# Kernel tuning notes

Measured on AMD Instinct MI355X. Metric: run time of the kernel, lower is better.

## Reference

```python
import jax, jax.numpy as jnp
import numpy as np

D = 768; NH = 12; DH = 64; DEPTH = 12; P = 16; IMG = 224; NC = 1000; DFF = 3072
GAMMA = 0.01; MIN_TOKENS = 16; EPS = 1e-6
SCALE = DH ** -0.5
NPATCH = (IMG // P) ** 2  # 196


def _ln(x, w, b, eps=1e-6):
    mu = x.mean(-1, keepdims=True)
    var = ((x - mu) ** 2).mean(-1, keepdims=True)
    return (x - mu) * jax.lax.rsqrt(var + eps) * w + b


def _block(x, p):
    # one pre-norm ViT block; returns new x, attention matrix A [B,H,T,T], values v [B,H,T,DH]
    (l1w, l1b, qw, qb, pw, pb, l2w, l2b, f1w, f1b, f2w, f2b) = p
    B, T, _ = x.shape
    qkv = _ln(x, l1w, l1b) @ qw + qb                      # [B,T,3D]
    qkv = qkv.reshape(B, T, 3, NH, DH).transpose(2, 0, 3, 1, 4)
    q, k, v = qkv[0], qkv[1], qkv[2]                      # [B,H,T,DH]
    A = jax.nn.softmax(jnp.einsum('bhtd,bhsd->bhts', q, k) * SCALE, axis=-1)
    out = jnp.einsum('bhts,bhsd->bhtd', A, v).transpose(0, 2, 1, 3).reshape(B, T, NH * DH)
    x = x + out @ pw + pb
    h = jax.nn.gelu(_ln(x, l2w, l2b) @ f1w + f1b, approximate=False)
    x = x + h @ f2w + f2b
    return x, A, v


def _embed(x, patch_w, patch_b, cls_token, pos_embed):
    B = x.shape[0]
    feat = jax.lax.conv_general_dilated(x, patch_w, (P, P), 'VALID',
                                        dimension_numbers=('NCHW', 'OIHW', 'NCHW'))  # [B,D,14,14]
    feat = feat.reshape(B, D, -1).transpose(0, 2, 1) + patch_b                       # [B,196,D]
    cls = jnp.broadcast_to(cls_token, (B, 1, D))
    return jnp.concatenate([cls, feat], axis=1) + pos_embed                          # [B,197,D]


def setup_inputs() -> dict:
    key = jax.random.key(0)
    ks = jax.random.split(key, 12)
    s = 0.02
    n = lambda k, shape: jax.random.normal(k, shape, jnp.float32) * s
    return {
        'x': jax.random.normal(ks[0], (32, 3, IMG, IMG), jnp.float32),
        'patch_w': n(ks[1], (D, 3, P, P)),
        'patch_b': jnp.zeros((D,), jnp.float32),
        'cls_token': n(ks[2], (1, 1, D)),
        'pos_embed': n(ks[3], (1, NPATCH + 1, D)),
        'ln1_w': jnp.ones((DEPTH, D), jnp.float32),
        'ln1_b': jnp.zeros((DEPTH, D), jnp.float32),
        'qkv_w': n(ks[4], (DEPTH, D, 3 * D)),
        'qkv_b': jnp.zeros((DEPTH, 3 * D), jnp.float32),
        'proj_w': n(ks[5], (DEPTH, D, D)),
        'proj_b': jnp.zeros((DEPTH, D), jnp.float32),
        'ln2_w': jnp.ones((DEPTH, D), jnp.float32),
        'ln2_b': jnp.zeros((DEPTH, D), jnp.float32),
        'fc1_w': n(ks[6], (DEPTH, D, DFF)),
        'fc1_b': jnp.zeros((DEPTH, DFF), jnp.float32),
        'fc2_w': n(ks[7], (DEPTH, DFF, D)),
        'fc2_b': jnp.zeros((DEPTH, D), jnp.float32),
        'norm_w': jnp.ones((D,), jnp.float32),
        'norm_b': jnp.zeros((D,), jnp.float32),
        'head_w': n(ks[8], (D, NC)),
        'head_b': jnp.zeros((NC,), jnp.float32),
    }


def reference(x, patch_w, patch_b, cls_token, pos_embed, ln1_w, ln1_b, qkv_w, qkv_b,
              proj_w, proj_b, ln2_w, ln2_b, fc1_w, fc1_b, fc2_w, fc2_b,
              norm_w, norm_b, head_w, head_b):
    # NOTE: token pruning produces data-dependent shapes, so this runs eagerly
    # (Python control flow on concrete values), exactly mirroring the torch code.
    x = _embed(x, patch_w, patch_b, cls_token, pos_embed)
    N = x.shape[1] - 1
    prev_mass = None
    for l in range(DEPTH):
        p = (ln1_w[l], ln1_b[l], qkv_w[l], qkv_b[l], proj_w[l], proj_b[l],
             ln2_w[l], ln2_b[l], fc1_w[l], fc1_b[l], fc2_w[l], fc2_b[l])
        x, A, v = _block(x, p)
        if N <= MIN_TOKENS:
            continue
        Am = A.mean(axis=1)                                   # [B,T,T] head-mean attention
        Vm = v.mean(axis=1)                                   # [B,T,DH] head-mean values
        rho = (1.0 + Am[:, 0, 0] * jnp.linalg.norm(Vm[:, 0], axis=-1)).mean()
        A_cls = Am[:, 0, 1:N + 1]                             # [B,N] cls->patch attention
        V_pt = Vm[:, 1:N + 1]
        Vc = V_pt - V_pt.mean(axis=1, keepdims=True)
        Vn = jnp.linalg.norm(Vc, axis=-1)                     # [B,N]
        mu = Vn.mean(axis=1, keepdims=True)
        sd = Vn.std(axis=1, keepdims=True, ddof=1)            # torch.std is unbiased
        J = A_cls * jax.nn.relu((Vn - mu) / (sd + EPS))       # [B,N] Jacobian score
        mass = J.sum(axis=1).mean()
        if prev_mass is not None:
            eta = mass / (prev_mass + EPS)
            keep_ratio = jnp.clip(rho * eta, 0.25, 4.0) ** (-GAMMA)
            N_next = max(MIN_TOKENS, int(N * float(keep_ratio)))
        else:
            N_next = N
        if N_next < N:
            idx = jnp.sort(jax.lax.top_k(J.mean(axis=0), N_next)[1]) + 1
            keep = jnp.concatenate([jnp.zeros((1,), idx.dtype), idx])
            x = x[:, keep]
            N = N_next
        prev_mass = mass
    x = _ln(x, norm_w, norm_b)
    return x[:, 0] @ head_w + head_b
```

## Files before the change

kernel.cpp:

```cpp
#include <hip/hip_runtime.h>
#include <math.h>

#define D 768
#define NH 12
#define DH 64
#define DEPTH 12
#define TMAX 197
#define NPATCH 196
#define BATCH 32
#define DFF 3072
#define NC 1000
#define QSTRIDE 2304
#define SCALE 0.125f
#define EPSF 1e-6f
#define MPAD 6400

typedef __bf16 bf16x8 __attribute__((ext_vector_type(8)));
typedef float f32x4 __attribute__((ext_vector_type(4)));
typedef short sshort8 __attribute__((ext_vector_type(8)));


__device__ __forceinline__ short f2bf(float x) {
  unsigned u = __float_as_uint(x);
  u = u + 0x7fffu + ((u >> 16) & 1u);
  return (short)(u >> 16);
}
__device__ __forceinline__ float bf2f(short h) {
  return __uint_as_float(((unsigned)(unsigned short)h) << 16);
}
__device__ __forceinline__ void bsplit(float x, short* hp, short* lp) {
  short h = f2bf(x);
  *hp = h;
  *lp = f2bf(x - bf2f(h));
}

__device__ __forceinline__ void gll16(const void* g, void* l) {
  __builtin_amdgcn_global_load_lds(
      (const __attribute__((address_space(1))) void*)g,
      (__attribute__((address_space(3))) void*)l, 16, 0, 0);
}


__device__ __forceinline__ float block_reduce_sum(float v, float* red, int tid) {
  red[tid] = v; __syncthreads();
  #pragma unroll
  for (int o = 128; o > 0; o >>= 1) { if (tid < o) red[tid] += red[tid + o]; __syncthreads(); }
  float r = red[0]; __syncthreads();
  return r;
}

__global__ void fail_kernel(float* out) { out[0] = 1.0e6f; }

__global__ void init_kernel(int* si, float* sf) {
  si[0] = TMAX;
  si[1] = 0;
  si[2] = 0;
  sf[0] = 0.f;
}

__global__ void wsplit_t(const float* __restrict__ W, short* __restrict__ Wpk,
                         int K, int N) {
  __shared__ float t[32][33];
  int n0 = blockIdx.x * 32, k0 = blockIdx.y * 32;
  int tid = threadIdx.x;
  int kk = tid >> 3, n4 = (tid & 7) * 4;
  float4 v = *(const float4*)(W + (size_t)(k0 + kk) * N + n0 + n4);
  t[kk][n4] = v.x; t[kk][n4 + 1] = v.y; t[kk][n4 + 2] = v.z; t[kk][n4 + 3] = v.w;
  __syncthreads();
  int nn = tid >> 3, k4 = (tid & 7) * 4;
  short* dh = Wpk + (size_t)(n0 + nn) * 2 * K + k0 + k4;
  short* dl = dh + K;
  #pragma unroll
  for (int c = 0; c < 4; ++c) bsplit(t[k4 + c][nn], &dh[c], &dl[c]);
}

__global__ void wsplit_nt(const float* __restrict__ W, short* __restrict__ Wpk, int K) {
  const float* src = W + (size_t)blockIdx.x * K;
  short* dh = Wpk + (size_t)blockIdx.x * 2 * K;
  short* dl = dh + K;
  for (int k = threadIdx.x; k < K; k += 256) bsplit(src[k], &dh[k], &dl[k]);
}


__global__ void im2col_kernel(const float* __restrict__ x, short* __restrict__ Impk) {
  int p = blockIdx.x, b = blockIdx.y;
  int py = p / 14, px = p % 14;
  short* dst = Impk + ((size_t)b * NPATCH + p) * 1536;
  for (int k = threadIdx.x; k < D; k += 256) {
    int c = k >> 8; int rem = k & 255; int i = rem >> 4; int j = rem & 15;
    float v = x[(((size_t)b * 3 + c) * 224 + py * 16 + i) * 224 + px * 16 + j];
    bsplit(v, &dst[k], &dst[768 + k]);
  }
}

__global__ void assemble_kernel(const float* __restrict__ PE, const float* __restrict__ cls,
                                const float* __restrict__ pos, float* __restrict__ X) {
  int t = blockIdx.x, b = blockIdx.y; int tid = threadIdx.x;
  float* xp = X + ((size_t)(b * TMAX) + t) * D;
  for (int k = tid; k < D; k += 256) {
    float v = (t == 0) ? cls[k] : PE[((size_t)(b * NPATCH) + (t - 1)) * D + k];
    xp[k] = v + pos[(size_t)t * D + k];
  }
}


__global__ void ln_kernel(const float* __restrict__ Xin, short* __restrict__ XNpk,
                          const float* __restrict__ wgt, const float* __restrict__ bsh,
                          const int* __restrict__ si) {
  int row = blockIdx.x;
  if ((row % TMAX) >= si[0]) return;
  __shared__ float red[256];
  int tid = threadIdx.x;
  const float* xp = Xin + (size_t)row * D;
  float v0 = xp[tid], v1 = xp[tid + 256], v2 = xp[tid + 512];
  float mu = block_reduce_sum(v0 + v1 + v2, red, tid) * (1.0f / 768.0f);
  float d0 = v0 - mu, d1 = v1 - mu, d2 = v2 - mu;
  float var = block_reduce_sum(d0 * d0 + d1 * d1 + d2 * d2, red, tid) * (1.0f / 768.0f);
  float inv = 1.0f / sqrtf(var + EPSF);
  short* op = XNpk + (size_t)row * 1536;
  float y0 = d0 * inv * wgt[tid] + bsh[tid];
  float y1 = d1 * inv * wgt[tid + 256] + bsh[tid + 256];
  float y2 = d2 * inv * wgt[tid + 512] + bsh[tid + 512];
  bsplit(y0, &op[tid], &op[768 + tid]);
  bsplit(y1, &op[tid + 256], &op[768 + tid + 256]);
  bsplit(y2, &op[tid + 512], &op[768 + tid + 512]);
}

__global__ void lnfinal_kernel(const float* __restrict__ X, float* __restrict__ CLSb,
                               const float* __restrict__ wgt, const float* __restrict__ bsh) {
  int b = blockIdx.x; int tid = threadIdx.x;
  __shared__ float red[256];
  const float* xp = X + (size_t)b * TMAX * D;
  float v0 = xp[tid], v1 = xp[tid + 256], v2 = xp[tid + 512];
  float mu = block_reduce_sum(v0 + v1 + v2, red, tid) * (1.0f / 768.0f);
  float d0 = v0 - mu, d1 = v1 - mu, d2 = v2 - mu;
  float var = block_reduce_sum(d0 * d0 + d1 * d1 + d2 * d2, red, tid) * (1.0f / 768.0f);
  float inv = 1.0f / sqrtf(var + EPSF);
  float* op = CLSb + (size_t)b * D;
  op[tid]       = d0 * inv * wgt[tid]       + bsh[tid];
  op[tid + 256] = d1 * inv * wgt[tid + 256] + bsh[tid + 256];
  op[tid + 512] = d2 * inv * wgt[tid + 512] + bsh[tid + 512];
}

__device__ __forceinline__ void swz_map(int d, int nx, int ny, int wsub,
                                        int& bx, int& by) {
  int q = ny >> 3, r = ny & 7;
  int rows, mb, l;
  int big = (q + 1) * nx;
  if (d < r * big) { int c = d / big; l = d - c * big; rows = q + 1; mb = c * (q + 1); }
  else { int d2 = d - r * big; int sm = q * nx; int c2 = d2 / sm; l = d2 - c2 * sm; rows = q; mb = r * (q + 1) + c2 * q; }
  int wspan = wsub * rows;
  int j = l / wspan; int t = l - j * wspan;
  int ml = t / wsub; int dx = t - ml * wsub;
  bx = j * wsub + dx; by = mb + ml;
}


#define GTM 128
#define GTN 128
#define GTK 32

template<int EPI, int SWZ>
__global__ __launch_bounds__(256)
void mgemm_kernel(const short* __restrict__ Apk, const short* __restrict__ Bpk,
                  const float* __restrict__ bias, const float* __restrict__ Rsrc,
                  float* __restrict__ Cf, short* __restrict__ Cpk,
                  int M, int K, int N, int nx, int ny, int wsub) {
  __shared__ char lds[65536];
  const int tid = threadIdx.x;
  const int ln = tid & 63;
  const int wv = tid >> 6;
  const int wm = wv >> 1, wn = wv & 1;

  int bx, by;
  if (SWZ) swz_map(blockIdx.x, nx, ny, wsub, bx, by);
  else { bx = blockIdx.x % nx; by = blockIdx.x / nx; }

  const int m0 = by * GTM, n0 = bx * GTN;
  const int lm = ln & 15, kc = ln >> 4;
  const size_t rs = 2 * (size_t)K;

  f32x4 acc[4][4];
  f32x4 zv = {0.f, 0.f, 0.f, 0.f};
  #pragma unroll
  for (int i = 0; i < 4; ++i)
    #pragma unroll
    for (int j = 0; j < 4; ++j) acc[i][j] = zv;

  auto stage = [&](int k0, int buf) {
    char* base = lds + (buf << 15);
    #pragma unroll
    for (int i = 0; i < 4; ++i) {
      int s = (i << 8) + tid;
      int r = s >> 3;
      int sl = (s & 7) ^ (r & 7);
      size_t eoff = (size_t)(sl >> 2) * K + (size_t)(k0 + ((sl & 3) << 3));
      int ldsoff = ((i << 8) + (tid & 192)) << 4;
      gll16(Apk + (size_t)(m0 + r) * rs + eoff, base + ldsoff);
      gll16(Bpk + (size_t)(n0 + r) * rs + eoff, base + 16384 + ldsoff);
    }
  };

  const int nk = K / GTK;
  stage(0, 0);
  for (int kt = 0; kt < nk; ++kt) {
    if (kt + 1 < nk) {
      stage((kt + 1) * GTK, (kt + 1) & 1);
      asm volatile("s_waitcnt vmcnt(8)" ::: "memory");
    } else {
      asm volatile("s_waitcnt vmcnt(0)" ::: "memory");
    }
    __builtin_amdgcn_s_barrier();
    __builtin_amdgcn_sched_barrier(0);

    const char* pa = lds + ((kt & 1) << 15);
    const char* pb = pa + 16384;
    bf16x8 bh[4], bl[4];
    #pragma unroll
    for (int j = 0; j < 4; ++j) {
      int c = wn * 64 + j * 16 + lm;
      int bo = c * 128 + ((kc ^ (c & 7)) << 4);
      bh[j] = *(const bf16x8*)(pb + bo);
      bl[j] = *(const bf16x8*)(pb + (bo ^ 64));
    }
    #pragma unroll
    for (int i = 0; i < 4; ++i) {
      int r = wm * 64 + i * 16 + lm;
      int ao = r * 128 + ((kc ^ (r & 7)) << 4);
      bf16x8 ah = *(const bf16x8*)(pa + ao);
      bf16x8 al = *(const bf16x8*)(pa + (ao ^ 64));
      #pragma unroll
      for (int j = 0; j < 4; ++j) {
        acc[i][j] = __builtin_amdgcn_mfma_f32_16x16x32_bf16(ah, bh[j], acc[i][j], 0, 0, 0);
        acc[i][j] = __builtin_amdgcn_mfma_f32_16x16x32_bf16(ah, bl[j], acc[i][j], 0, 0, 0);
        acc[i][j] = __builtin_amdgcn_mfma_f32_16x16x32_bf16(al, bh[j], acc[i][j], 0, 0, 0);
      }
    }
    if (kt + 1 < nk)
      __builtin_amdgcn_s_barrier();
  }

  #pragma unroll
  for (int i = 0; i < 4; ++i) {
    #pragma unroll
    for (int t = 0; t < 4; ++t) {
      int m = m0 + wm * 64 + i * 16 + kc * 4 + t;
      if (m >= M) continue;
      #pragma unroll
      for (int j = 0; j < 4; ++j) {
        int n = n0 + wn * 64 + j * 16 + lm;
        float v = acc[i][j][t] + bias[n];
        if (EPI == 1) v += Rsrc[(size_t)m * N + n];
        if (EPI == 2) {
          v = v * 0.5f * (1.0f + erff(v * 0.70710678118654752f));
          short h = f2bf(v);
          Cpk[(size_t)m * 2 * N + n] = h;
          Cpk[(size_t)m * 2 * N + N + n] = f2bf(v - bf2f(h));
        } else {
          Cf[(size_t)m * N + n] = v;
        }
      }
    }
  }
}


#define BM 128
#define BN 64
#define BK 16

__global__ __launch_bounds__(256, 2)
void gemm_kernel(const float* __restrict__ A, const float* __restrict__ Bw,
                 const float* __restrict__ bias, float* __restrict__ C,
                 int M, int K, int N) {
  __shared__ float As[BK][BM + 4];
  __shared__ float Bs[BK][BN];
  int tid = threadIdx.x;
  int tx = tid & 15;
  int ty = tid >> 4;
  int m0 = blockIdx.y * BM;
  int n0 = blockIdx.x * BN;
  float acc[8][4];
  #pragma unroll
  for (int i = 0; i < 8; ++i)
    #pragma unroll
    for (int j = 0; j < 4; ++j) acc[i][j] = 0.f;
  const int lkA = tid & 15;
  const int lmA = tid >> 4;
  const int lnB = tid & 63;
  const int lkB = tid >> 6;
  for (int k0 = 0; k0 < K; k0 += BK) {
    #pragma unroll
    for (int r = 0; r < 8; ++r) {
      int ml = r * 16 + lmA;
      int m = m0 + ml;
      float va = 0.f;
      if (m < M) va = A[(size_t)m * K + k0 + lkA];
      As[lkA][ml] = va;
    }
    #pragma unroll
    for (int r = 0; r < 4; ++r) {
      int kk = r * 4 + lkB;
      int n = n0 + lnB;
      float vb = 0.f;
      if (n < N) vb = Bw[(size_t)(k0 + kk) * N + n];
      Bs[kk][lnB] = vb;
    }
    __syncthreads();
    #pragma unroll
    for (int kk = 0; kk < BK; ++kk) {
      const float4 b4 = *(const float4*)(&Bs[kk][tx * 4]);
      const float4 a0 = *(const float4*)(&As[kk][ty * 8]);
      const float4 a1 = *(const float4*)(&As[kk][ty * 8 + 4]);
      const float a[8] = {a0.x, a0.y, a0.z, a0.w, a1.x, a1.y, a1.z, a1.w};
      const float bb[4] = {b4.x, b4.y, b4.z, b4.w};
      #pragma unroll
      for (int i = 0; i < 8; ++i)
        #pragma unroll
        for (int j = 0; j < 4; ++j)
          acc[i][j] = fmaf(a[i], bb[j], acc[i][j]);
    }
    __syncthreads();
  }
  #pragma unroll
  for (int i = 0; i < 8; ++i) {
    int m = m0 + ty * 8 + i;
    if (m >= M) continue;
    #pragma unroll
    for (int j = 0; j < 4; ++j) {
      int n = n0 + tx * 4 + j;
      if (n >= N) continue;
      C[(size_t)m * N + n] = acc[i][j] + bias[n];
    }
  }
}


#define QT 64
#define KVT 64

__global__ __launch_bounds__(256)
void mattn_kernel(const float* __restrict__ QKV, short* __restrict__ AOpk,
                  const int* __restrict__ si) {
  const int tok = si[0];
  const int bh = blockIdx.x; const int b = bh / NH, h = bh % NH;
  const int q0 = blockIdx.y * QT;
  if (q0 >= tok) return;
  __shared__ short Kh[4096], Kl[4096], Vth[4096], Vtl[4096];
  __shared__ short Pb[8192];
  const int tid = threadIdx.x;
  const int l = tid & 63, w = tid >> 6;
  const int lm = l & 15, lg = l >> 4;

  bf16x8 qh[2], ql[2];
  {
    int qrow = q0 + w * 16 + lm;
    if (qrow >= TMAX) qrow = TMAX - 1;
    const float* qp = QKV + (size_t)(b * TMAX + qrow) * QSTRIDE + h * DH + lg * 8;
    #pragma unroll
    for (int c = 0; c < 2; ++c) {
      sshort8 hs, ls;
      #pragma unroll
      for (int j = 0; j < 8; ++j) {
        float v = qp[c * 32 + j];
        short hh = f2bf(v);
        hs[j] = hh;
        ls[j] = f2bf(v - bf2f(hh));
      }
      qh[c] = __builtin_bit_cast(bf16x8, hs);
      ql[c] = __builtin_bit_cast(bf16x8, ls);
    }
  }

  float mrun[4], lrun[4];
  f32x4 oacc[4];
  f32x4 zv = {0.f, 0.f, 0.f, 0.f};
  #pragma unroll
  for (int t = 0; t < 4; ++t) { mrun[t] = -1e30f; lrun[t] = 0.f; }
  #pragma unroll
  for (int j = 0; j < 4; ++j) oacc[j] = zv;

  const int r0 = (tid >> 4) * 4;
  const int td4 = (tid & 15) * 4;

  for (int j0 = 0; j0 < tok; j0 += KVT) {
    {
      float vbuf[16];
      #pragma unroll
      for (int i = 0; i < 4; ++i) {
        int gr = j0 + r0 + i; if (gr >= TMAX) gr = TMAX - 1;
        const float* kp = QKV + (size_t)(b * TMAX + gr) * QSTRIDE + D + h * DH + td4;
        float4 kv = *(const float4*)kp;
        short4 sh, sl;
        sh.x = f2bf(kv.x); sl.x = f2bf(kv.x - bf2f(sh.x));
        sh.y = f2bf(kv.y); sl.y = f2bf(kv.y - bf2f(sh.y));
        sh.z = f2bf(kv.z); sl.z = f2bf(kv.z - bf2f(sh.z));
        sh.w = f2bf(kv.w); sl.w = f2bf(kv.w - bf2f(sh.w));
        int r = r0 + i;
        int so = r * 64 + (((td4 >> 3) ^ (r & 7)) << 3) + (td4 & 7);
        *(short4*)(Kh + so) = sh;
        *(short4*)(Kl + so) = sl;
        const float* vp = QKV + (size_t)(b * TMAX + gr) * QSTRIDE + 2 * D + h * DH + td4;
        float4 vv = *(const float4*)vp;
        vbuf[i * 4 + 0] = vv.x; vbuf[i * 4 + 1] = vv.y;
        vbuf[i * 4 + 2] = vv.z; vbuf[i * 4 + 3] = vv.w;
      }
      #pragma unroll
      for (int dd = 0; dd < 4; ++dd) {
        int d = td4 + dd;
        short4 sh, sl;
        float c0 = vbuf[dd], c1 = vbuf[4 + dd], c2 = vbuf[8 + dd], c3 = vbuf[12 + dd];
        sh.x = f2bf(c0); sl.x = f2bf(c0 - bf2f(sh.x));
        sh.y = f2bf(c1); sl.y = f2bf(c1 - bf2f(sh.y));
        sh.z = f2bf(c2); sl.z = f2bf(c2 - bf2f(sh.z));
        sh.w = f2bf(c3); sl.w = f2bf(c3 - bf2f(sh.w));
        int so = d * 64 + (((r0 >> 3) ^ (d & 7)) << 3) + (r0 & 7);
        *(short4*)(Vth + so) = sh;
        *(short4*)(Vtl + so) = sl;
      }
    }
    __syncthreads();

    f32x4 sacc[4];
    #pragma unroll
    for (int jk = 0; jk < 4; ++jk) sacc[jk] = zv;
    #pragma unroll
    for (int c = 0; c < 2; ++c) {
      #pragma unroll
      for (int jk = 0; jk < 4; ++jk) {
        int row = jk * 16 + lm;
        int so = row * 64 + (((c * 4 + lg) ^ (row & 7)) << 3);
        bf16x8 kbh = *(const bf16x8*)(Kh + so);
        bf16x8 kbl = *(const bf16x8*)(Kl + so);
        sacc[jk] = __builtin_amdgcn_mfma_f32_16x16x32_bf16(qh[c], kbh, sacc[jk], 0, 0, 0);
        sacc[jk] = __builtin_amdgcn_mfma_f32_16x16x32_bf16(qh[c], kbl, sacc[jk], 0, 0, 0);
        sacc[jk] = __builtin_amdgcn_mfma_f32_16x16x32_bf16(ql[c], kbh, sacc[jk], 0, 0, 0);
      }
    }

    float p[4][4];
    #pragma unroll
    for (int jk = 0; jk < 4; ++jk) {
      bool valid = (j0 + jk * 16 + lm) < tok;
      #pragma unroll
      for (int t = 0; t < 4; ++t)
        p[jk][t] = valid ? sacc[jk][t] * SCALE : -1e30f;
    }
    float mt[4], mnew[4], co[4], rsm[4];
    #pragma unroll
    for (int t = 0; t < 4; ++t) {
      mt[t] = fmaxf(fmaxf(p[0][t], p[1][t]), fmaxf(p[2][t], p[3][t]));
      #pragma unroll
      for (int off = 1; off < 16; off <<= 1)
        mt[t] = fmaxf(mt[t], __shfl_xor(mt[t], off, 16));
      mnew[t] = fmaxf(mrun[t], mt[t]);
      co[t] = expf(mrun[t] - mnew[t]);
      rsm[t] = 0.f;
    }
    #pragma unroll
    for (int jk = 0; jk < 4; ++jk)
      #pragma unroll
      for (int t = 0; t < 4; ++t) {
        p[jk][t] = expf(p[jk][t] - mnew[t]);
        rsm[t] += p[jk][t];
      }
    #pragma unroll
    for (int t = 0; t < 4; ++t) {
      #pragma unroll
      for (int off = 1; off < 16; off <<= 1)
        rsm[t] += __shfl_xor(rsm[t], off, 16);
      lrun[t] = lrun[t] * co[t] + rsm[t];
      mrun[t] = mnew[t];
    }
    #pragma unroll
    for (int jd = 0; jd < 4; ++jd)
      #pragma unroll
      for (int t = 0; t < 4; ++t) oacc[jd][t] *= co[t];

    short* Pw = Pb + w * 2048;
    #pragma unroll
    for (int jk = 0; jk < 4; ++jk)
      #pragma unroll
      for (int t = 0; t < 4; ++t) {
        int q = lg * 4 + t;
        int col = jk * 16 + lm;
        short hh = f2bf(p[jk][t]);
        short hl = f2bf(p[jk][t] - bf2f(hh));
        int so = q * 64 + (((col >> 3) ^ (q & 7)) << 3) + (col & 7);
        Pw[so] = hh;
        Pw[1024 + so] = hl;
      }

    #pragma unroll
    for (int c = 0; c < 2; ++c) {
      int aro = lm * 64 + (((c * 4 + lg) ^ (lm & 7)) << 3);
      bf16x8 pah = *(const bf16x8*)(Pw + aro);
      bf16x8 pal = *(const bf16x8*)(Pw + 1024 + aro);
      #pragma unroll
      for (int jd = 0; jd < 4; ++jd) {
        int d = jd * 16 + lm;
        int so = d * 64 + (((c * 4 + lg) ^ (d & 7)) << 3);
        bf16x8 vbh = *(const bf16x8*)(Vth + so);
        bf16x8 vbl = *(const bf16x8*)(Vtl + so);
        oacc[jd] = __builtin_amdgcn_mfma_f32_16x16x32_bf16(pah, vbh, oacc[jd], 0, 0, 0);
        oacc[jd] = __builtin_amdgcn_mfma_f32_16x16x32_bf16(pah, vbl, oacc[jd], 0, 0, 0);
        oacc[jd] = __builtin_amdgcn_mfma_f32_16x16x32_bf16(pal, vbh, oacc[jd], 0, 0, 0);
      }
    }
    __syncthreads();
  }

  #pragma unroll
  for (int t = 0; t < 4; ++t) {
    int q = q0 + w * 16 + lg * 4 + t;
    if (q >= tok) continue;
    float inv = 1.0f / lrun[t];
    short* op = AOpk + (size_t)(b * TMAX + q) * 1536 + h * DH;
    #pragma unroll
    for (int jd = 0; jd < 4; ++jd) {
      int d = jd * 16 + lm;
      float y = oacc[jd][t] * inv;
      short hh = f2bf(y);
      op[d] = hh;
      op[768 + d] = f2bf(y - bf2f(hh));
    }
  }
}

__global__ void clsrow_kernel(const float* __restrict__ QKV, float* __restrict__ Pcls,
                              const int* __restrict__ si) {
  int tok = si[0];
  int bh = blockIdx.x; int b = bh / NH, h = bh % NH;
  int tid = threadIdx.x;
  __shared__ float q[DH];
  __shared__ float red[256];
  if (tid < DH) q[tid] = QKV[((size_t)(b * TMAX)) * QSTRIDE + h * DH + tid];
  __syncthreads();
  float sval = -1e30f;
  if (tid < tok) {
    const float* kp = QKV + ((size_t)(b * TMAX) + tid) * QSTRIDE + D + h * DH;
    float a = 0.f;
    #pragma unroll
    for (int dd = 0; dd < DH; ++dd) a = fmaf(q[dd], kp[dd], a);
    sval = a * SCALE;
  }
  red[tid] = sval; __syncthreads();
  #pragma unroll
  for (int o = 128; o > 0; o >>= 1) { if (tid < o) red[tid] = fmaxf(red[tid], red[tid + o]); __syncthreads(); }
  float mx = red[0]; __syncthreads();
  float e = (tid < tok) ? expf(sval - mx) : 0.f;
  red[tid] = e; __syncthreads();
  #pragma unroll
  for (int o = 128; o > 0; o >>= 1) { if (tid < o) red[tid] += red[tid + o]; __syncthreads(); }
  if (tid < tok) Pcls[(size_t)bh * TMAX + tid] = e / red[0];
}

__global__ void aclsmean_kernel(const float* __restrict__ Pcls, float* __restrict__ Acls,
                                const int* __restrict__ si) {
  int tok = si[0]; int b = blockIdx.x; int tid = threadIdx.x;
  if (tid < tok) {
    float s = 0.f;
    #pragma unroll
    for (int h = 0; h < NH; ++h) s += Pcls[((size_t)b * NH + h) * TMAX + tid];
    Acls[b * TMAX + tid] = s * (1.0f / 12.0f);
  }
}

__global__ void vmean_kernel(const float* __restrict__ QKV, float* __restrict__ Vm,
                             const int* __restrict__ si) {
  int tok = si[0];
  int t = blockIdx.x, b = blockIdx.y;
  if (t >= tok) return;
  int d = threadIdx.x;
  const float* vp = QKV + ((size_t)(b * TMAX + t)) * QSTRIDE + 2 * D;
  float s = 0.f;
  #pragma unroll
  for (int h = 0; h < NH; ++h) s += vp[h * DH + d];
  Vm[((size_t)b * TMAX + t) * DH + d] = s * (1.0f / 12.0f);
}


__global__ void stats_kernel(const float* __restrict__ Vm, const float* __restrict__ Acls,
                             float* __restrict__ Jbuf, float* __restrict__ Jsum,
                             float* __restrict__ rhot, const int* __restrict__ si) {
  int tok = si[0]; int N = tok - 1;
  if (N <= 16) return;
  int b = blockIdx.x; int tid = threadIdx.x;
  __shared__ float red[256];
  __shared__ float vmean[DH];
  __shared__ float Vn[NPATCH];
  const float* vb = Vm + (size_t)b * TMAX * DH;

  float x0 = 0.f;
  if (tid < DH) { float v = vb[tid]; x0 = v * v; }
  red[tid] = x0; __syncthreads();
  #pragma unroll
  for (int o = 128; o > 0; o >>= 1) { if (tid < o) red[tid] += red[tid + o]; __syncthreads(); }
  if (tid == 0) rhot[b] = 1.0f + Acls[b * TMAX] * sqrtf(red[0]);
  __syncthreads();

  int d = tid & 63, part = tid >> 6;
  float s = 0.f;
  for (int t = 1 + part; t <= N; t += 4) s += vb[(size_t)t * DH + d];
  red[tid] = s; __syncthreads();
  if (tid < DH) vmean[tid] = (red[tid] + red[tid + 64] + red[tid + 128] + red[tid + 192]) / (float)N;
  __syncthreads();

  if (tid < N) {
    const float* vp = vb + (size_t)(tid + 1) * DH;
    float a = 0.f;
    #pragma unroll
    for (int dd = 0; dd < DH; ++dd) { float z = vp[dd] - vmean[dd]; a = fmaf(z, z, a); }
    Vn[tid] = sqrtf(a);
  }
  __syncthreads();

  red[tid] = (tid < N) ? Vn[tid] : 0.f; __syncthreads();
  #pragma unroll
  for (int o = 128; o > 0; o >>= 1) { if (tid < o) red[tid] += red[tid + o]; __syncthreads(); }
  float mu = red[0] / (float)N;
  __syncthreads();
  float dv = (tid < N) ? (Vn[tid] - mu) : 0.f;
  red[tid] = dv * dv; __syncthreads();
  #pragma unroll
  for (int o = 128; o > 0; o >>= 1) { if (tid < o) red[tid] += red[tid + o]; __syncthreads(); }
  float sd = sqrtf(red[0] / (float)(N - 1));
  __syncthreads();

  float Jv = 0.f;
  if (tid < N) {
    float z = (Vn[tid] - mu) / (sd + EPSF);
    z = fmaxf(z, 0.f);
    Jv = Acls[b * TMAX + 1 + tid] * z;
    Jbuf[b * NPATCH + tid] = Jv;
  }
  red[tid] = Jv; __syncthreads();
  #pragma unroll
  for (int o = 128; o > 0; o >>= 1) { if (tid < o) red[tid] += red[tid + o]; __syncthreads(); }
  if (tid == 0) Jsum[b] = red[0];
}

__global__ void decide_kernel(const float* __restrict__ Jbuf, const float* __restrict__ Jsum,
                              const float* __restrict__ rhot, int* __restrict__ keep,
                              int* __restrict__ si, float* __restrict__ sf) {
  int tok = si[0]; int N = tok - 1;
  int tid = threadIdx.x;
  if (N <= 16) { if (tid == 0) si[2] = 0; return; }
  __shared__ float red[256];
  __shared__ float Jms[NPATCH];
  __shared__ int sel[NPATCH];

  red[tid] = (tid < BATCH) ? rhot[tid] : 0.f; __syncthreads();
  #pragma unroll
  for (int o = 128; o > 0; o >>= 1) { if (tid < o) red[tid] += red[tid + o]; __syncthreads(); }
  float rho = red[0] / (float)BATCH; __syncthreads();
  red[tid] = (tid < BATCH) ? Jsum[tid] : 0.f; __syncthreads();
  #pragma unroll
  for (int o = 128; o > 0; o >>= 1) { if (tid < o) red[tid] += red[tid + o]; __syncthreads(); }
  float mass = red[0] / (float)BATCH;
  int prev_valid = si[1];
  float prev = sf[0];
  __syncthreads();

  int N_next = N;
  if (prev_valid) {
    float eta = mass / (prev + EPSF);
    float re = rho * eta;
    re = fminf(fmaxf(re, 0.25f), 4.0f);
    double kr = pow((double)re, -0.01);
    int nn = (int)((double)N * kr);
    N_next = nn > 16 ? nn : 16;
  }
  if (tid == 0) { si[1] = 1; sf[0] = mass; }

  if (N_next < N) {
    if (tid < N) {
      float sJ = 0.f;
      for (int bb = 0; bb < BATCH; ++bb) sJ += Jbuf[bb * NPATCH + tid];
      Jms[tid] = sJ / (float)BATCH;
    }
    __syncthreads();
    if (tid < N) {
      float me = Jms[tid]; int rank = 0;
      for (int s2 = 0; s2 < N; ++s2) {
        float ov = Jms[s2];
        if (ov > me || (ov == me && s2 < tid)) ++rank;
      }
      sel[tid] = (rank < N_next) ? 1 : 0;
    }
    __syncthreads();
    if (tid == 0) {
      int c = 0; keep[c++] = 0;
      for (int t2 = 0; t2 < N; ++t2) if (sel[t2]) keep[c++] = t2 + 1;
      si[0] = N_next + 1;
      si[2] = 1;
    }
  } else {
    if (tid == 0) si[2] = 0;
  }
}

__global__ void gather_kernel(const float* __restrict__ X, float* __restrict__ T,
                              const int* __restrict__ keep, const int* __restrict__ si) {
  if (!si[2]) return;
  int tok = si[0];
  int i = blockIdx.x, b = blockIdx.y;
  if (i >= tok) return;
  int src = keep[i];
  const float* xp = X + ((size_t)(b * TMAX) + src) * D;
  float* tp = T + ((size_t)(b * TMAX) + i) * D;
  int tid = threadIdx.x;
  tp[tid] = xp[tid]; tp[tid + 256] = xp[tid + 256]; tp[tid + 512] = xp[tid + 512];
}

__global__ void copyback_kernel(const float* __restrict__ T, float* __restrict__ X,
                                const int* __restrict__ si) {
  if (!si[2]) return;
  int tok = si[0];
  int i = blockIdx.x, b = blockIdx.y;
  if (i >= tok) return;
  const float* tp = T + ((size_t)(b * TMAX) + i) * D;
  float* xp = X + ((size_t)(b * TMAX) + i) * D;
  int tid = threadIdx.x;
  xp[tid] = tp[tid]; xp[tid + 256] = tp[tid + 256]; xp[tid + 512] = tp[tid + 512];
}


extern "C" void kernel_launch(void* const* d_in, const int* in_sizes, int n_in,
                              void* d_out, int out_size, void* d_ws, size_t ws_size,
                              hipStream_t stream) {
  (void)in_sizes; (void)n_in; (void)out_size;
  const float* x       = (const float*)d_in[0];
  const float* patch_w = (const float*)d_in[1];
  const float* patch_b = (const float*)d_in[2];
  const float* cls_tok = (const float*)d_in[3];
  const float* pos     = (const float*)d_in[4];
  const float* ln1w    = (const float*)d_in[5];
  const float* ln1b    = (const float*)d_in[6];
  const float* qkvw    = (const float*)d_in[7];
  const float* qkvb    = (const float*)d_in[8];
  const float* projw   = (const float*)d_in[9];
  const float* projb   = (const float*)d_in[10];
  const float* ln2w    = (const float*)d_in[11];
  const float* ln2b    = (const float*)d_in[12];
  const float* fc1w    = (const float*)d_in[13];
  const float* fc1b    = (const float*)d_in[14];
  const float* fc2w    = (const float*)d_in[15];
  const float* fc2b    = (const float*)d_in[16];
  const float* normw   = (const float*)d_in[17];
  const float* normb   = (const float*)d_in[18];
  const float* headw   = (const float*)d_in[19];
  const float* headb   = (const float*)d_in[20];
  float* out = (float*)d_out;

  char* w = (char*)d_ws;
  size_t off = 0;
  auto alloc = [&](size_t bytes) -> void* {
    void* p = w + off;
    off += (bytes + 255) & ~(size_t)255;
    return p;
  };
  const size_t MROWS = (size_t)BATCH * TMAX;
  float* X    = (float*)alloc(MROWS * D * 4);
  short* XNpk = (short*)alloc((size_t)MPAD * 1536 * 2);
  float* QKV  = (float*)alloc(MROWS * QSTRIDE * 4);
  short* AOpk = (short*)alloc((size_t)MPAD * 1536 * 2);
  short* Hpk  = (short*)alloc((size_t)MPAD * 2 * DFF * 2);
  float* Vm   = (float*)alloc(MROWS * DH * 4);
  float* Pcls = (float*)alloc((size_t)BATCH * NH * TMAX * 4);
  float* Acls = (float*)alloc((size_t)BATCH * TMAX * 4);
  float* Jbuf = (float*)alloc((size_t)BATCH * NPATCH * 4);
  float* Jsum = (float*)alloc(BATCH * 4);
  float* rhot = (float*)alloc(BATCH * 4);
  int*   keep = (int*)alloc(256 * 4);
  int*   si   = (int*)alloc(64 * 4);
  float* sf   = (float*)alloc(64 * 4);
  float* CLS  = (float*)alloc((size_t)BATCH * D * 4);
  short* Wq   = (short*)alloc((size_t)QSTRIDE * 2 * D * 2);
  short* Wp   = (short*)alloc((size_t)D * 2 * D * 2);
  short* W1   = (short*)alloc((size_t)DFF * 2 * D * 2);
  short* W2   = (short*)alloc((size_t)D * 2 * DFF * 2);
  short* Wpat = (short*)alloc((size_t)D * 2 * D * 2);
  short* Impk = Hpk;
  float* TMP  = (float*)Hpk;
  float* Ef32 = QKV;

  if (off > ws_size) {
    fail_kernel<<<1, 1, 0, stream>>>(out);
    return;
  }

  init_kernel<<<1, 1, 0, stream>>>(si, sf);

  im2col_kernel<<<dim3(NPATCH, BATCH), 256, 0, stream>>>(x, Impk);
  wsplit_nt<<<D, 256, 0, stream>>>(patch_w, Wpat, D);
  mgemm_kernel<0, 1><<<6 * 49, 256, 0, stream>>>(
      Impk, Wpat, patch_b, nullptr, Ef32, nullptr, BATCH * NPATCH, D, D, 6, 49, 6);
  assemble_kernel<<<dim3(TMAX, BATCH), 256, 0, stream>>>(Ef32, cls_tok, pos, X);

  for (int l = 0; l < DEPTH; ++l) {
    const float* l1w = ln1w + l * D;
    const float* l1b = ln1b + l * D;
    const float* qw  = qkvw + (size_t)l * D * 3 * D;
    const float* qb  = qkvb + (size_t)l * 3 * D;
    const float* pw  = projw + (size_t)l * D * D;
    const float* pb  = projb + (size_t)l * D;
    const float* l2w = ln2w + l * D;
    const float* l2b = ln2b + l * D;
    const float* f1w = fc1w + (size_t)l * D * DFF;
    const float* f1b = fc1b + (size_t)l * DFF;
    const float* f2w = fc2w + (size_t)l * DFF * D;
    const float* f2b = fc2b + (size_t)l * D;

    wsplit_t<<<dim3(QSTRIDE / 32, D / 32), 256, 0, stream>>>(qw, Wq, D, QSTRIDE);
    wsplit_t<<<dim3(D / 32, D / 32), 256, 0, stream>>>(pw, Wp, D, D);
    wsplit_t<<<dim3(DFF / 32, D / 32), 256, 0, stream>>>(f1w, W1, D, DFF);
    wsplit_t<<<dim3(D / 32, DFF / 32), 256, 0, stream>>>(f2w, W2, DFF, D);

    ln_kernel<<<BATCH * TMAX, 256, 0, stream>>>(X, XNpk, l1w, l1b, si);
    mgemm_kernel<0, 1><<<18 * 50, 256, 0, stream>>>(
        XNpk, Wq, qb, nullptr, QKV, nullptr, (int)MROWS, D, QSTRIDE, 18, 50, 6);
    mattn_kernel<<<dim3(BATCH * NH, (TMAX + QT - 1) / QT), 256, 0, stream>>>(QKV, AOpk, si);
    clsrow_kernel<<<BATCH * NH, 256, 0, stream>>>(QKV, Pcls, si);
    aclsmean_kernel<<<BATCH, 256, 0, stream>>>(Pcls, Acls, si);
    vmean_kernel<<<dim3(TMAX, BATCH), 64, 0, stream>>>(QKV, Vm, si);
    mgemm_kernel<1, 1><<<6 * 50, 256, 0, stream>>>(
        AOpk, Wp, pb, X, X, nullptr, (int)MROWS, D, D, 6, 50, 6);
    ln_kernel<<<BATCH * TMAX, 256, 0, stream>>>(X, XNpk, l2w, l2b, si);
    mgemm_kernel<2, 1><<<24 * 50, 256, 0, stream>>>(
        XNpk, W1, f1b, nullptr, nullptr, Hpk, (int)MROWS, D, DFF, 24, 50, 8);
    mgemm_kernel<1, 0><<<6 * 50, 256, 0, stream>>>(
        Hpk, W2, f2b, X, X, nullptr, (int)MROWS, DFF, D, 6, 50, 6);
    stats_kernel<<<BATCH, 256, 0, stream>>>(Vm, Acls, Jbuf, Jsum, rhot, si);
    decide_kernel<<<1, 256, 0, stream>>>(Jbuf, Jsum, rhot, keep, si, sf);
    gather_kernel<<<dim3(TMAX, BATCH), 256, 0, stream>>>(X, TMP, keep, si);
    copyback_kernel<<<dim3(TMAX, BATCH), 256, 0, stream>>>(TMP, X, si);
  }

  lnfinal_kernel<<<BATCH, 256, 0, stream>>>(X, CLS, normw, normb);
  gemm_kernel<<<dim3(16, 1), 256, 0, stream>>>(CLS, headw, headb, out, BATCH, D, NC);
}
```

Before: 6.730 ms.

## Emit QKV as pre-split bf16 hi/lo pairs and simplify GEMM pipeline sync

The QKV GEMM gains a new epilogue that writes each output as a bf16 hi/lo pair. The attention, cls-row and v-mean kernels then read those pairs directly instead of splitting fp32 values on every load. The GEMM main loop also swaps its hand-placed vmcnt waits and split barriers for a single __syncthreads before staging the next tile, which may reduce how much load latency overlaps with compute. Clsrow and vmean now rebuild fp32 from hi+lo, a small precision change. The embedding output buffer is aliased onto AOpk.

```diff
diff --git a/kernel.cpp b/kernel.cpp
--- a/kernel.cpp
+++ b/kernel.cpp
@@ -11,6 +11,7 @@
 #define DFF 3072
 #define NC 1000
 #define QSTRIDE 2304
+#define QPK 4608
 #define SCALE 0.125f
 #define EPSF 1e-6f
 #define MPAD 6400
@@ -204,15 +205,8 @@
   const int nk = K / GTK;
   stage(0, 0);
   for (int kt = 0; kt < nk; ++kt) {
-    if (kt + 1 < nk) {
-      stage((kt + 1) * GTK, (kt + 1) & 1);
-      asm volatile("s_waitcnt vmcnt(8)" ::: "memory");
-    } else {
-      asm volatile("s_waitcnt vmcnt(0)" ::: "memory");
-    }
-    __builtin_amdgcn_s_barrier();
-    __builtin_amdgcn_sched_barrier(0);
-
+    __syncthreads();
+    if (kt + 1 < nk) stage((kt + 1) * GTK, (kt + 1) & 1);
     const char* pa = lds + ((kt & 1) << 15);
     const char* pb = pa + 16384;
     bf16x8 bh[4], bl[4];
@@ -236,8 +230,6 @@
         acc[i][j] = __builtin_amdgcn_mfma_f32_16x16x32_bf16(al, bh[j], acc[i][j], 0, 0, 0);
       }
     }
-    if (kt + 1 < nk)
-      __builtin_amdgcn_s_barrier();
   }
 
   #pragma unroll
@@ -251,8 +243,8 @@
         int n = n0 + wn * 64 + j * 16 + lm;
         float v = acc[i][j][t] + bias[n];
         if (EPI == 1) v += Rsrc[(size_t)m * N + n];
-        if (EPI == 2) {
-          v = v * 0.5f * (1.0f + erff(v * 0.70710678118654752f));
+        if (EPI == 2 || EPI == 3) {
+          if (EPI == 2) v = v * 0.5f * (1.0f + erff(v * 0.70710678118654752f));
           short h = f2bf(v);
           Cpk[(size_t)m * 2 * N + n] = h;
           Cpk[(size_t)m * 2 * N + N + n] = f2bf(v - bf2f(h));
@@ -340,7 +332,7 @@
 #define KVT 64
 
 __global__ __launch_bounds__(256)
-void mattn_kernel(const float* __restrict__ QKV, short* __restrict__ AOpk,
+void mattn_kernel(const short* __restrict__ QKVpk, short* __restrict__ AOpk,
                   const int* __restrict__ si) {
   const int tok = si[0];
   const int bh = blockIdx.x; const int b = bh / NH, h = bh % NH;
@@ -356,19 +348,11 @@
   {
     int qrow = q0 + w * 16 + lm;
     if (qrow >= TMAX) qrow = TMAX - 1;
-    const float* qp = QKV + (size_t)(b * TMAX + qrow) * QSTRIDE + h * DH + lg * 8;
+    const short* qp = QKVpk + (size_t)(b * TMAX + qrow) * QPK + h * DH + lg * 8;
     #pragma unroll
     for (int c = 0; c < 2; ++c) {
-      sshort8 hs, ls;
-      #pragma unroll
-      for (int j = 0; j < 8; ++j) {
-        float v = qp[c * 32 + j];
-        short hh = f2bf(v);
-        hs[j] = hh;
-        ls[j] = f2bf(v - bf2f(hh));
-      }
-      qh[c] = __builtin_bit_cast(bf16x8, hs);
-      ql[c] = __builtin_bit_cast(bf16x8, ls);
+      qh[c] = __builtin_bit_cast(bf16x8, *(const sshort8*)(qp + c * 32));
+      ql[c] = __builtin_bit_cast(bf16x8, *(const sshort8*)(qp + QSTRIDE + c * 32));
     }
   }
 
@@ -385,35 +369,28 @@
 
   for (int j0 = 0; j0 < tok; j0 += KVT) {
     {
-      float vbuf[16];
+      short vh[16], vl[16];
       #pragma unroll
       for (int i = 0; i < 4; ++i) {
         int gr = j0 + r0 + i; if (gr >= TMAX) gr = TMAX - 1;
-        const float* kp = QKV + (size_t)(b * TMAX + gr) * QSTRIDE + D + h * DH + td4;
-        float4 kv = *(const float4*)kp;
-        short4 sh, sl;
-        sh.x = f2bf(kv.x); sl.x = f2bf(kv.x - bf2f(sh.x));
-        sh.y = f2bf(kv.y); sl.y = f2bf(kv.y - bf2f(sh.y));
-        sh.z = f2bf(kv.z); sl.z = f2bf(kv.z - bf2f(sh.z));
-        sh.w = f2bf(kv.w); sl.w = f2bf(kv.w - bf2f(sh.w));
+        const short* bp = QKVpk + (size_t)(b * TMAX + gr) * QPK;
+        short4 kh4 = *(const short4*)(bp + D + h * DH + td4);
+        short4 kl4 = *(const short4*)(bp + D + QSTRIDE + h * DH + td4);
         int r = r0 + i;
         int so = r * 64 + (((td4 >> 3) ^ (r & 7)) << 3) + (td4 & 7);
-        *(short4*)(Kh + so) = sh;
-        *(short4*)(Kl + so) = sl;
-        const float* vp = QKV + (size_t)(b * TMAX + gr) * QSTRIDE + 2 * D + h * DH + td4;
-        float4 vv = *(const float4*)vp;
-        vbuf[i * 4 + 0] = vv.x; vbuf[i * 4 + 1] = vv.y;
-        vbuf[i * 4 + 2] = vv.z; vbuf[i * 4 + 3] = vv.w;
+        *(short4*)(Kh + so) = kh4;
+        *(short4*)(Kl + so) = kl4;
+        short4 vh4 = *(const short4*)(bp + 2 * D + h * DH + td4);
+        short4 vl4 = *(const short4*)(bp + 2 * D + QSTRIDE + h * DH + td4);
+        vh[i * 4 + 0] = vh4.x; vh[i * 4 + 1] = vh4.y; vh[i * 4 + 2] = vh4.z; vh[i * 4 + 3] = vh4.w;
+        vl[i * 4 + 0] = vl4.x; vl[i * 4 + 1] = vl4.y; vl[i * 4 + 2] = vl4.z; vl[i * 4 + 3] = vl4.w;
       }
       #pragma unroll
       for (int dd = 0; dd < 4; ++dd) {
         int d = td4 + dd;
         short4 sh, sl;
-        float c0 = vbuf[dd], c1 = vbuf[4 + dd], c2 = vbuf[8 + dd], c3 = vbuf[12 + dd];
-        sh.x = f2bf(c0); sl.x = f2bf(c0 - bf2f(sh.x));
-        sh.y = f2bf(c1); sl.y = f2bf(c1 - bf2f(sh.y));
-        sh.z = f2bf(c2); sl.z = f2bf(c2 - bf2f(sh.z));
-        sh.w = f2bf(c3); sl.w = f2bf(c3 - bf2f(sh.w));
+        sh.x = vh[dd]; sh.y = vh[4 + dd]; sh.z = vh[8 + dd]; sh.w = vh[12 + dd];
+        sl.x = vl[dd]; sl.y = vl[4 + dd]; sl.z = vl[8 + dd]; sl.w = vl[12 + dd];
         int so = d * 64 + (((r0 >> 3) ^ (d & 7)) << 3) + (r0 & 7);
         *(short4*)(Vth + so) = sh;
         *(short4*)(Vtl + so) = sl;
@@ -527,21 +504,25 @@
   }
 }
 
-__global__ void clsrow_kernel(const float* __restrict__ QKV, float* __restrict__ Pcls,
+__global__ void clsrow_kernel(const short* __restrict__ QKVpk, float* __restrict__ Pcls,
                               const int* __restrict__ si) {
   int tok = si[0];
   int bh = blockIdx.x; int b = bh / NH, h = bh % NH;
   int tid = threadIdx.x;
   __shared__ float q[DH];
   __shared__ float red[256];
-  if (tid < DH) q[tid] = QKV[((size_t)(b * TMAX)) * QSTRIDE + h * DH + tid];
+  if (tid < DH) {
+    const short* qp = QKVpk + (size_t)(b * TMAX) * QPK + h * DH;
+    q[tid] = bf2f(qp[tid]) + bf2f(qp[QSTRIDE + tid]);
+  }
   __syncthreads();
   float sval = -1e30f;
   if (tid < tok) {
-    const float* kp = QKV + ((size_t)(b * TMAX) + tid) * QSTRIDE + D + h * DH;
+    const short* kp = QKVpk + ((size_t)(b * TMAX) + tid) * QPK + D + h * DH;
     float a = 0.f;
     #pragma unroll
-    for (int dd = 0; dd < DH; ++dd) a = fmaf(q[dd], kp[dd], a);
+    for (int dd = 0; dd < DH; ++dd)
+      a = fmaf(q[dd], bf2f(kp[dd]) + bf2f(kp[QSTRIDE + dd]), a);
     sval = a * SCALE;
   }
   red[tid] = sval; __syncthreads();
@@ -566,16 +547,17 @@
   }
 }
 
-__global__ void vmean_kernel(const float* __restrict__ QKV, float* __restrict__ Vm,
+__global__ void vmean_kernel(const short* __restrict__ QKVpk, float* __restrict__ Vm,
                              const int* __restrict__ si) {
   int tok = si[0];
   int t = blockIdx.x, b = blockIdx.y;
   if (t >= tok) return;
   int d = threadIdx.x;
-  const float* vp = QKV + ((size_t)(b * TMAX + t)) * QSTRIDE + 2 * D;
+  const short* vp = QKVpk + ((size_t)(b * TMAX + t)) * QPK + 2 * D;
   float s = 0.f;
   #pragma unroll
-  for (int h = 0; h < NH; ++h) s += vp[h * DH + d];
+  for (int h = 0; h < NH; ++h)
+    s += bf2f(vp[h * DH + d]) + bf2f(vp[QSTRIDE + h * DH + d]);
   Vm[((size_t)b * TMAX + t) * DH + d] = s * (1.0f / 12.0f);
 }
 
@@ -761,29 +743,29 @@
     return p;
   };
   const size_t MROWS = (size_t)BATCH * TMAX;
-  float* X    = (float*)alloc(MROWS * D * 4);
-  short* XNpk = (short*)alloc((size_t)MPAD * 1536 * 2);
-  float* QKV  = (float*)alloc(MROWS * QSTRIDE * 4);
-  short* AOpk = (short*)alloc((size_t)MPAD * 1536 * 2);
-  short* Hpk  = (short*)alloc((size_t)MPAD * 2 * DFF * 2);
-  float* Vm   = (float*)alloc(MROWS * DH * 4);
-  float* Pcls = (float*)alloc((size_t)BATCH * NH * TMAX * 4);
-  float* Acls = (float*)alloc((size_t)BATCH * TMAX * 4);
-  float* Jbuf = (float*)alloc((size_t)BATCH * NPATCH * 4);
-  float* Jsum = (float*)alloc(BATCH * 4);
-  float* rhot = (float*)alloc(BATCH * 4);
-  int*   keep = (int*)alloc(256 * 4);
-  int*   si   = (int*)alloc(64 * 4);
-  float* sf   = (float*)alloc(64 * 4);
-  float* CLS  = (float*)alloc((size_t)BATCH * D * 4);
-  short* Wq   = (short*)alloc((size_t)QSTRIDE * 2 * D * 2);
-  short* Wp   = (short*)alloc((size_t)D * 2 * D * 2);
-  short* W1   = (short*)alloc((size_t)DFF * 2 * D * 2);
-  short* W2   = (short*)alloc((size_t)D * 2 * DFF * 2);
-  short* Wpat = (short*)alloc((size_t)D * 2 * D * 2);
-  short* Impk = Hpk;
-  float* TMP  = (float*)Hpk;
-  float* Ef32 = QKV;
+  float* X     = (float*)alloc(MROWS * D * 4);
+  short* XNpk  = (short*)alloc((size_t)MPAD * 1536 * 2);
+  short* QKVpk = (short*)alloc(MROWS * QPK * 2);
+  short* AOpk  = (short*)alloc((size_t)MPAD * 1536 * 2);
+  short* Hpk   = (short*)alloc((size_t)MPAD * 2 * DFF * 2);
+  float* Vm    = (float*)alloc(MROWS * DH * 4);
+  float* Pcls  = (float*)alloc((size_t)BATCH * NH * TMAX * 4);
+  float* Acls  = (float*)alloc((size_t)BATCH * TMAX * 4);
+  float* Jbuf  = (float*)alloc((size_t)BATCH * NPATCH * 4);
+  float* Jsum  = (float*)alloc(BATCH * 4);
+  float* rhot  = (float*)alloc(BATCH * 4);
+  int*   keep  = (int*)alloc(256 * 4);
+  int*   si    = (int*)alloc(64 * 4);
+  float* sf    = (float*)alloc(64 * 4);
+  float* CLS   = (float*)alloc((size_t)BATCH * D * 4);
+  short* Wq    = (short*)alloc((size_t)QSTRIDE * 2 * D * 2);
+  short* Wp    = (short*)alloc((size_t)D * 2 * D * 2);
+  short* W1    = (short*)alloc((size_t)DFF * 2 * D * 2);
+  short* W2    = (short*)alloc((size_t)D * 2 * DFF * 2);
+  short* Wpat  = (short*)alloc((size_t)D * 2 * D * 2);
+  short* Impk  = Hpk;
+  float* TMP   = (float*)Hpk;
+  float* Ef32  = (float*)AOpk;
 
   if (off > ws_size) {
     fail_kernel<<<1, 1, 0, stream>>>(out);
@@ -818,12 +800,12 @@
     wsplit_t<<<dim3(D / 32, DFF / 32), 256, 0, stream>>>(f2w, W2, DFF, D);
 
     ln_kernel<<<BATCH * TMAX, 256, 0, stream>>>(X, XNpk, l1w, l1b, si);
-    mgemm_kernel<0, 1><<<18 * 50, 256, 0, stream>>>(
-        XNpk, Wq, qb, nullptr, QKV, nullptr, (int)MROWS, D, QSTRIDE, 18, 50, 6);
-    mattn_kernel<<<dim3(BATCH * NH, (TMAX + QT - 1) / QT), 256, 0, stream>>>(QKV, AOpk, si);
-    clsrow_kernel<<<BATCH * NH, 256, 0, stream>>>(QKV, Pcls, si);
+    mgemm_kernel<3, 1><<<18 * 50, 256, 0, stream>>>(
+        XNpk, Wq, qb, nullptr, nullptr, QKVpk, (int)MROWS, D, QSTRIDE, 18, 50, 6);
+    mattn_kernel<<<dim3(BATCH * NH, (TMAX + QT - 1) / QT), 256, 0, stream>>>(QKVpk, AOpk, si);
+    clsrow_kernel<<<BATCH * NH, 256, 0, stream>>>(QKVpk, Pcls, si);
     aclsmean_kernel<<<BATCH, 256, 0, stream>>>(Pcls, Acls, si);
-    vmean_kernel<<<dim3(TMAX, BATCH), 64, 0, stream>>>(QKV, Vm, si);
+    vmean_kernel<<<dim3(TMAX, BATCH), 64, 0, stream>>>(QKVpk, Vm, si);
     mgemm_kernel<1, 1><<<6 * 50, 256, 0, stream>>>(
         AOpk, Wp, pb, X, X, nullptr, (int)MROWS, D, D, 6, 50, 6);
     ln_kernel<<<BATCH * TMAX, 256, 0, stream>>>(X, XNpk, l2w, l2b, si);
```

Result: faster. 6.545 ms (-2.8%).
